# Kernel tuning notes

Hardware: AMD Instinct MI355X
Metric: run time of the kernel (lower is better)

Reference implementation:

```python
import jax, jax.numpy as jnp
import numpy as np

N = 100000
E = 1600000
G = 100
HEADS = 4
CH = 32
POS = 16
IN_DIM = 128
OUT_DIM = 64
NEG_SLOPE = 0.2
BN_EPS = 1e-5


def _grid_positions(batch):
    # replicate _get_normalized_positions: per-graph ceil(sqrt(count)) grid, vectorized
    counts = jax.ops.segment_sum(jnp.ones(N, jnp.int32), batch, num_segments=G)
    starts = jnp.concatenate([jnp.zeros(1, jnp.int32), jnp.cumsum(counts)[:-1].astype(jnp.int32)])
    local = jnp.arange(N, dtype=jnp.int32) - starts[batch]
    cnt = counts[batch]
    gs = jnp.ceil(jnp.sqrt(cnt.astype(jnp.float32))).astype(jnp.int32)
    row = local // gs
    col = local % gs
    denom = jnp.maximum(gs - 1, 1).astype(jnp.float32)
    return jnp.stack([row.astype(jnp.float32) / denom, col.astype(jnp.float32) / denom], axis=1)


def _seg_softmax(alpha, dst):
    # numerically-stable softmax over edges grouped by destination node
    amax = jax.ops.segment_max(alpha, dst, num_segments=N)
    amax = jnp.where(jnp.isfinite(amax), amax, 0.0)
    e = jnp.exp(alpha - amax[dst])
    s = jax.ops.segment_sum(e, dst, num_segments=N)
    return e / (s[dst] + 1e-16)


def _gat_layer(h, pos, src, dst, W, att, Wp, b):
    xt = (h @ W.T).reshape(N, HEADS, CH)                       # [N,H,C]
    pe = (pos[dst] - pos[src]) @ Wp.T                          # [E',P]
    a = att[0]                                                 # [H, 2C+P]
    # decompose (cat(x_src, x_dst, pe) * att).sum(-1) to avoid [E',H,2C+P] intermediate
    a_src = jnp.einsum('nhc,hc->nh', xt, a[:, :CH])
    a_dst = jnp.einsum('nhc,hc->nh', xt, a[:, CH:2 * CH])
    alpha = a_src[src] + a_dst[dst] + pe @ a[:, 2 * CH:].T     # [E',H]
    alpha = jnp.where(alpha > 0, alpha, NEG_SLOPE * alpha)     # leaky_relu
    alpha = _seg_softmax(alpha, dst)
    # faithful to source: message uses x[dst_idx], aggregated onto dst
    out = jax.ops.segment_sum(xt[dst] * alpha[:, :, None], dst, num_segments=N)
    return out.reshape(N, HEADS * CH) + b


def _batchnorm(h, g, b):
    mu = h.mean(0)
    var = h.var(0)  # biased, matches torch BN training-mode normalization
    return (h - mu) / jnp.sqrt(var + BN_EPS) * g + b


def setup_inputs() -> dict:
    key = jax.random.key(0)
    ks = jax.random.split(key, 20)
    s = 0.1
    return {
        'x': jax.random.normal(ks[0], (N, IN_DIM), jnp.float32),
        'edge_index': jax.random.randint(ks[1], (2, E), 0, N, jnp.int32),
        'batch': (jnp.arange(N, dtype=jnp.int32) // (N // G)).astype(jnp.int32),
        'pe_W': jax.random.normal(ks[2], (POS, 2), jnp.float32) * s,
        'pe_b': jax.random.normal(ks[3], (POS,), jnp.float32) * s,
        'lin_W0': jax.random.normal(ks[4], (HEADS * CH, IN_DIM + POS), jnp.float32) * s,
        'att0': jax.random.normal(ks[5], (1, HEADS, 2 * CH + POS), jnp.float32) * s,
        'posW0': jax.random.normal(ks[6], (POS, 2), jnp.float32) * s,
        'bias0': jax.random.normal(ks[7], (HEADS * CH,), jnp.float32) * s,
        'bn_g0': jax.random.uniform(ks[8], (HEADS * CH,), jnp.float32, 0.5, 1.5),
        'bn_b0': jax.random.normal(ks[9], (HEADS * CH,), jnp.float32) * s,
        'lin_W1': jax.random.normal(ks[10], (HEADS * CH, HEADS * CH), jnp.float32) * s,
        'att1': jax.random.normal(ks[11], (1, HEADS, 2 * CH + POS), jnp.float32) * s,
        'posW1': jax.random.normal(ks[12], (POS, 2), jnp.float32) * s,
        'bias1': jax.random.normal(ks[13], (HEADS * CH,), jnp.float32) * s,
        'bn_g1': jax.random.uniform(ks[14], (HEADS * CH,), jnp.float32, 0.5, 1.5),
        'bn_b1': jax.random.normal(ks[15], (HEADS * CH,), jnp.float32) * s,
        'fc_W': jax.random.normal(ks[16], (OUT_DIM, HEADS * CH), jnp.float32) * s,
        'fc_b': jax.random.normal(ks[17], (OUT_DIM,), jnp.float32) * s,
    }


def reference(x, edge_index, batch, pe_W, pe_b,
              lin_W0, att0, posW0, bias0, bn_g0, bn_b0,
              lin_W1, att1, posW1, bias1, bn_g1, bn_b1,
              fc_W, fc_b):
    pos = _grid_positions(batch)
    h = jnp.concatenate([x, pos @ pe_W.T + pe_b], axis=1)      # PositionalEncoding
    loop = jnp.arange(N, dtype=edge_index.dtype)
    src = jnp.concatenate([edge_index[0], loop])               # add_self_loops
    dst = jnp.concatenate([edge_index[1], loop])
    layers = ((lin_W0, att0, posW0, bias0, bn_g0, bn_b0),
              (lin_W1, att1, posW1, bias1, bn_g1, bn_b1))
    for (W, att, Wp, b, g, bb) in layers:
        h = _gat_layer(h, pos, src, dst, W, att, Wp, b)
        h = _batchnorm(h, g, bb)
        h = jax.nn.elu(h)
        # dropout: eval mode (identity); _refine_positions is identity
    counts = jax.ops.segment_sum(jnp.ones(N, jnp.float32), batch, num_segments=G)
    pooled = jax.ops.segment_sum(h, batch, num_segments=G) / counts[:, None]
    return pooled @ fc_W.T + fc_b
```

## Files before the change

kernel.cpp:

```cpp
#include <hip/hip_runtime.h>

#define NN 100000

typedef __bf16 bf16x8 __attribute__((ext_vector_type(8)));
typedef float  f32x4  __attribute__((ext_vector_type(4)));

__device__ __forceinline__ float b2f(ushort u) {
    union { unsigned int i; float f; } v; v.i = ((unsigned int)u) << 16; return v.f;
}
__device__ __forceinline__ ushort f2b(float f) {
    union { float f; unsigned int i; } v; v.f = f;
    unsigned int r = (v.i + 0x7fffu + ((v.i >> 16) & 1u)) >> 16;
    return (ushort)r;
}
__device__ __forceinline__ float elu_f(float v) {
    return v > 0.0f ? v : __expf(v) - 1.0f;
}

__global__ __launch_bounds__(256)
void zero_k(const float* __restrict__ W0, const float* __restrict__ W1,
            float* __restrict__ stats, float* __restrict__ out,
            ushort* __restrict__ wb0, ushort* __restrict__ wb1) {
    int i = blockIdx.x * 256 + threadIdx.x;
    if (i < 14592) { if (i < 8192) stats[i] = 0.0f; else out[i - 8192] = 0.0f; }
    if (i < 18432) wb0[i] = f2b(W0[i]);
    else if (i < 34816) wb1[i - 18432] = f2b(W1[i - 18432]);
}

template<int KK, int KP, bool FIRST>
__global__ __launch_bounds__(256, 4)
void gemm_k(const void* __restrict__ Av, const ushort* __restrict__ Wb,
            const float* __restrict__ peW, const float* __restrict__ peB,
            const float* __restrict__ statsIn, const float* __restrict__ g,
            const float* __restrict__ bb, ushort* __restrict__ Z,
            float* __restrict__ statsOut)
{
    constexpr int NKC = KP / 32;
    __shared__ ushort ZS[64 * 136];
    __shared__ float smS[256], smQ[256];
    __shared__ float smSS[256];
    const int t = threadIdx.x;
    const int blockM = blockIdx.x * 64;

    const int wave = t >> 6, lane = t & 63;
    const int wm = (wave & 1) * 32, wn = (wave >> 1) * 64;
    const int m = lane & 15, kq = lane >> 4;

    bf16x8 af[2][NKC];
    if constexpr (FIRST) {
        const float* A = (const float*)Av;
        #pragma unroll
        for (int mi = 0; mi < 2; ++mi) {
            const int gr = blockM + wm + mi * 16 + m;
            const bool ok = gr < NN;
            #pragma unroll
            for (int kc = 0; kc < 4; ++kc) {
                const int k0 = kc * 32 + kq * 8;
                float4 v0 = make_float4(0.f, 0.f, 0.f, 0.f), v1 = v0;
                if (ok) {
                    v0 = *(const float4*)(A + (size_t)gr * 128 + k0);
                    v1 = *(const float4*)(A + (size_t)gr * 128 + k0 + 4);
                }
                ushort u[8] = { f2b(v0.x), f2b(v0.y), f2b(v0.z), f2b(v0.w),
                                f2b(v1.x), f2b(v1.y), f2b(v1.z), f2b(v1.w) };
                af[mi][kc] = *(bf16x8*)u;
            }
            {
                ushort u[8] = {0, 0, 0, 0, 0, 0, 0, 0};
                if (kq < 2 && ok) {
                    const int local = gr - (gr / 1000) * 1000;
                    const float px = (float)(local >> 5) * (1.0f / 31.0f);
                    const float py = (float)(local & 31) * (1.0f / 31.0f);
                    #pragma unroll
                    for (int j = 0; j < 8; ++j) {
                        int p = kq * 8 + j;
                        u[j] = f2b(px * peW[2 * p] + py * peW[2 * p + 1] + peB[p]);
                    }
                }
                af[mi][NKC - 1] = *(bf16x8*)u;
            }
        }
    } else {
        const ushort* A = (const ushort*)Av;
        uint4 raw[2][4];
        #pragma unroll
        for (int mi = 0; mi < 2; ++mi) {
            const int gr = blockM + wm + mi * 16 + m;
            const bool ok = gr < NN;
            #pragma unroll
            for (int kc = 0; kc < 4; ++kc) {
                raw[mi][kc] = make_uint4(0u, 0u, 0u, 0u);
                if (ok) raw[mi][kc] = *(const uint4*)(A + (size_t)gr * 128 + kc * 32 + kq * 8);
            }
        }
        if (t < 128) {
            float S = 0.f, Q = 0.f;
            #pragma unroll
            for (int k = 0; k < 16; ++k) {
                S += statsIn[k * 256 + t]; Q += statsIn[k * 256 + 128 + t];
            }
            float mu = S * (1.0f / NN);
            float var = fmaxf(Q * (1.0f / NN) - mu * mu, 0.0f);
            float istd = rsqrtf(var + 1e-5f);
            float sc = g[t] * istd;
            smSS[t] = sc; smSS[128 + t] = bb[t] - mu * sc;
        }
        __syncthreads();
        #pragma unroll
        for (int mi = 0; mi < 2; ++mi) {
            const bool ok = (blockM + wm + mi * 16 + m) < NN;
            #pragma unroll
            for (int kc = 0; kc < 4; ++kc) {
                const int k0 = kc * 32 + kq * 8;
                ushort* u = (ushort*)&raw[mi][kc];
                #pragma unroll
                for (int j = 0; j < 8; ++j) {
                    float val = b2f(u[j]) * smSS[k0 + j] + smSS[128 + k0 + j];
                    u[j] = ok ? f2b(elu_f(val)) : (ushort)0;
                }
                af[mi][kc] = *(bf16x8*)&raw[mi][kc];
            }
        }
    }

    f32x4 acc[2][4];
    #pragma unroll
    for (int mi = 0; mi < 2; ++mi)
        #pragma unroll
        for (int ni = 0; ni < 4; ++ni)
            acc[mi][ni] = (f32x4){0.0f, 0.0f, 0.0f, 0.0f};

    #pragma unroll
    for (int kc = 0; kc < NKC; ++kc) {
        const int k0 = kc * 32 + kq * 8;
        bf16x8 bf[4];
        #pragma unroll
        for (int ni = 0; ni < 4; ++ni) {
            if (KP == KK || k0 < KK)
                bf[ni] = *(const bf16x8*)(Wb + (wn + ni * 16 + m) * KK + k0);
            else {
                ushort z[8] = {0, 0, 0, 0, 0, 0, 0, 0};
                bf[ni] = *(bf16x8*)z;
            }
        }
        #pragma unroll
        for (int mi = 0; mi < 2; ++mi)
            #pragma unroll
            for (int ni = 0; ni < 4; ++ni)
                acc[mi][ni] = __builtin_amdgcn_mfma_f32_16x16x32_bf16(
                    af[mi][kc], bf[ni], acc[mi][ni], 0, 0, 0);
    }

    float s[4] = {0, 0, 0, 0}, q[4] = {0, 0, 0, 0};
    #pragma unroll
    for (int mi = 0; mi < 2; ++mi)
        #pragma unroll
        for (int ni = 0; ni < 4; ++ni)
            #pragma unroll
            for (int r = 0; r < 4; ++r) {
                const float z = acc[mi][ni][r];
                s[ni] += z; q[ni] += z * z;
            }
    #pragma unroll
    for (int ni = 0; ni < 4; ++ni) {
        s[ni] += __shfl_xor(s[ni], 16); s[ni] += __shfl_xor(s[ni], 32);
        q[ni] += __shfl_xor(q[ni], 16); q[ni] += __shfl_xor(q[ni], 32);
    }
    if (lane < 16) {
        #pragma unroll
        for (int ni = 0; ni < 4; ++ni) {
            const int idx = wave * 64 + ni * 16 + m;
            smS[idx] = s[ni]; smQ[idx] = q[ni];
        }
    }
    #pragma unroll
    for (int mi = 0; mi < 2; ++mi)
        #pragma unroll
        for (int ni = 0; ni < 4; ++ni) {
            const int col = wn + ni * 16 + m;
            const int rb = wm + mi * 16 + kq * 4;
            #pragma unroll
            for (int r = 0; r < 4; ++r)
                ZS[(rb + r) * 136 + col] = f2b(acc[mi][ni][r]);
        }
    __syncthreads();

    if (t < 128) {
        const int base = (t >> 6) * 128 + (t & 63);
        float S = smS[base] + smS[base + 64];
        float Q = smQ[base] + smQ[base + 64];
        float* sl = statsOut + (blockIdx.x & 15) * 256;
        atomicAdd(sl + t, S);
        atomicAdd(sl + 128 + t, Q);
    }
    #pragma unroll
    for (int i = 0; i < 4; ++i) {
        const int idx = i * 256 + t;
        const int row = idx >> 4, c16 = idx & 15;
        const int gr = blockM + row;
        if (gr < NN)
            *(uint4*)(Z + (size_t)gr * 128 + c16 * 8) =
                *(const uint4*)(ZS + row * 136 + c16 * 8);
    }
}

__global__ __launch_bounds__(256)
void poolfc_k(const ushort* __restrict__ Z, const float* __restrict__ stats,
              const float* __restrict__ g, const float* __restrict__ bb,
              const float* __restrict__ fcW, const float* __restrict__ fcB,
              float* __restrict__ out) {
    __shared__ float smSS[256];
    __shared__ float smT[16 * 128];
    __shared__ float smP[128];
    const int t = threadIdx.x;
    if (t < 128) {
        float S = 0.f, Q = 0.f;
        #pragma unroll
        for (int k = 0; k < 16; ++k) { S += stats[k * 256 + t]; Q += stats[k * 256 + 128 + t]; }
        float mu = S * (1.0f / NN);
        float var = fmaxf(Q * (1.0f / NN) - mu * mu, 0.0f);
        float istd = rsqrtf(var + 1e-5f);
        float sc = g[t] * istd;
        smSS[t] = sc; smSS[128 + t] = bb[t] - mu * sc;
    }
    __syncthreads();
    const int gg = blockIdx.x >> 2, part = blockIdx.x & 3;
    const int r16 = t >> 4, c8 = t & 15;
    const int r0 = gg * 1000 + part * 250;
    float sc[8], sh[8];
    #pragma unroll
    for (int j = 0; j < 8; ++j) { sc[j] = smSS[c8 * 8 + j]; sh[j] = smSS[128 + c8 * 8 + j]; }
    float a[8] = {0, 0, 0, 0, 0, 0, 0, 0};
    #pragma unroll
    for (int i = 0; i < 16; ++i) {
        if (i < 15 || r16 < 10) {
            const uint4 v = *(const uint4*)(Z + ((size_t)(r0 + i * 16 + r16)) * 128 + c8 * 8);
            const ushort* u = (const ushort*)&v;
            #pragma unroll
            for (int j = 0; j < 8; ++j) a[j] += elu_f(b2f(u[j]) * sc[j] + sh[j]);
        }
    }
    #pragma unroll
    for (int j = 0; j < 8; ++j) smT[r16 * 128 + c8 * 8 + j] = a[j];
    __syncthreads();
    if (t < 128) {
        float S = 0.0f;
        #pragma unroll
        for (int k = 0; k < 16; ++k) S += smT[k * 128 + t];
        smP[t] = S;
    }
    __syncthreads();
    if (t < 64) {
        float d = 0.0f;
        #pragma unroll
        for (int j4 = 0; j4 < 32; ++j4) {
            float4 w = *(const float4*)(fcW + t * 128 + j4 * 4);
            d += smP[j4 * 4 + 0] * w.x + smP[j4 * 4 + 1] * w.y
               + smP[j4 * 4 + 2] * w.z + smP[j4 * 4 + 3] * w.w;
        }
        float acc = d * (1.0f / 1000.0f) + (part == 0 ? fcB[t] : 0.0f);
        atomicAdd(&out[gg * 64 + t], acc);
    }
}

extern "C" void kernel_launch(void* const* d_in, const int* in_sizes, int n_in,
                              void* d_out, int out_size, void* d_ws, size_t ws_size,
                              hipStream_t stream) {
    const float* x   = (const float*)d_in[0];
    const float* peW = (const float*)d_in[3];
    const float* peB = (const float*)d_in[4];
    const float* W0  = (const float*)d_in[5];
    const float* g0  = (const float*)d_in[9];
    const float* bb0 = (const float*)d_in[10];
    const float* W1  = (const float*)d_in[11];
    const float* g1  = (const float*)d_in[15];
    const float* bb1 = (const float*)d_in[16];
    const float* fcW = (const float*)d_in[17];
    const float* fcB = (const float*)d_in[18];
    float* out = (float*)d_out;

    float* wsF = (float*)d_ws;
    float* stats1 = wsF;
    float* stats2 = wsF + 4096;
    ushort* wb0 = (ushort*)((char*)d_ws + 65536);
    ushort* wb1 = (ushort*)((char*)d_ws + 131072);
    ushort* z1 = (ushort*)((char*)d_ws + 262144);
    ushort* z2 = (ushort*)((char*)d_ws + 25862144);

    zero_k<<<136, 256, 0, stream>>>(W0, W1, stats1, out, wb0, wb1);
    gemm_k<144, 160, true ><<<1563, 256, 0, stream>>>(
        (const void*)x, wb0, peW, peB, nullptr, nullptr, nullptr, z1, stats1);
    gemm_k<128, 128, false><<<1563, 256, 0, stream>>>(
        (const void*)z1, wb1, nullptr, nullptr, stats1, g0, bb0, z2, stats2);
    poolfc_k<<<400, 256, 0, stream>>>(z2, stats2, g1, bb1, fcW, fcB, out);
}
```

Baseline: 183.8 us.

## Recompute first GEMM to fuse BN+ELU into second GEMM, dropping intermediate buffer

Result: slower. 190.9 us (+3.9%).

```diff
diff --git a/kernel.cpp b/kernel.cpp
--- a/kernel.cpp
+++ b/kernel.cpp
@@ -27,152 +27,209 @@
     else if (i < 34816) wb1[i - 18432] = f2b(W1[i - 18432]);
 }
 
-template<int KK, int KP, bool FIRST>
-__global__ __launch_bounds__(256, 4)
-void gemm_k(const void* __restrict__ Av, const ushort* __restrict__ Wb,
-            const float* __restrict__ peW, const float* __restrict__ peB,
-            const float* __restrict__ statsIn, const float* __restrict__ g,
-            const float* __restrict__ bb, ushort* __restrict__ Z,
-            float* __restrict__ statsOut)
+__device__ __forceinline__ void build_af(bf16x8 af[2][5], const float* __restrict__ x,
+                                         const float* __restrict__ peW,
+                                         const float* __restrict__ peB,
+                                         int blockM, int wm, int m, int kq) {
+    #pragma unroll
+    for (int mi = 0; mi < 2; ++mi) {
+        const int gr = blockM + wm + mi * 16 + m;
+        const bool ok = gr < NN;
+        #pragma unroll
+        for (int kc = 0; kc < 4; ++kc) {
+            const int k0 = kc * 32 + kq * 8;
+            float4 v0 = make_float4(0.f, 0.f, 0.f, 0.f), v1 = v0;
+            if (ok) {
+                v0 = *(const float4*)(x + (size_t)gr * 128 + k0);
+                v1 = *(const float4*)(x + (size_t)gr * 128 + k0 + 4);
+            }
+            ushort u[8] = { f2b(v0.x), f2b(v0.y), f2b(v0.z), f2b(v0.w),
+                            f2b(v1.x), f2b(v1.y), f2b(v1.z), f2b(v1.w) };
+            af[mi][kc] = *(bf16x8*)u;
+        }
+        {
+            ushort u[8] = {0, 0, 0, 0, 0, 0, 0, 0};
+            if (kq < 2 && ok) {
+                const int local = gr - (gr / 1000) * 1000;
+                const float px = (float)(local >> 5) * (1.0f / 31.0f);
+                const float py = (float)(local & 31) * (1.0f / 31.0f);
+                #pragma unroll
+                for (int j = 0; j < 8; ++j) {
+                    int p = kq * 8 + j;
+                    u[j] = f2b(px * peW[2 * p] + py * peW[2 * p + 1] + peB[p]);
+                }
+            }
+            af[mi][4] = *(bf16x8*)u;
+        }
+    }
+}
+
+__device__ __forceinline__ void mfma_s1(f32x4 acc[2][4], bf16x8 af[2][5],
+                                        const ushort* __restrict__ wb0,
+                                        int wn, int m, int kq) {
+    #pragma unroll
+    for (int kc = 0; kc < 5; ++kc) {
+        const int k0 = kc * 32 + kq * 8;
+        bf16x8 bf[4];
+        #pragma unroll
+        for (int ni = 0; ni < 4; ++ni) {
+            if (k0 < 144)
+                bf[ni] = *(const bf16x8*)(wb0 + (wn + ni * 16 + m) * 144 + k0);
+            else {
+                ushort z[8] = {0, 0, 0, 0, 0, 0, 0, 0};
+                bf[ni] = *(bf16x8*)z;
+            }
+        }
+        #pragma unroll
+        for (int mi = 0; mi < 2; ++mi)
+            #pragma unroll
+            for (int ni = 0; ni < 4; ++ni)
+                acc[mi][ni] = __builtin_amdgcn_mfma_f32_16x16x32_bf16(
+                    af[mi][kc], bf[ni], acc[mi][ni], 0, 0, 0);
+    }
+}
+
+__device__ __forceinline__ void stats_epi(const f32x4 acc[2][4], float* smS, float* smQ,
+                                          float* __restrict__ statsOut,
+                                          int t, int wave, int lane, int wn, int m,
+                                          int bid) {
+    float s[4] = {0, 0, 0, 0}, q[4] = {0, 0, 0, 0};
+    #pragma unroll
+    for (int mi = 0; mi < 2; ++mi)
+        #pragma unroll
+        for (int ni = 0; ni < 4; ++ni)
+            #pragma unroll
+            for (int r = 0; r < 4; ++r) {
+                const float z = acc[mi][ni][r];
+                s[ni] += z; q[ni] += z * z;
+            }
+    #pragma unroll
+    for (int ni = 0; ni < 4; ++ni) {
+        s[ni] += __shfl_xor(s[ni], 16); s[ni] += __shfl_xor(s[ni], 32);
+        q[ni] += __shfl_xor(q[ni], 16); q[ni] += __shfl_xor(q[ni], 32);
+    }
+    if (lane < 16) {
+        #pragma unroll
+        for (int ni = 0; ni < 4; ++ni) {
+            const int idx = wave * 64 + ni * 16 + m;
+            smS[idx] = s[ni]; smQ[idx] = q[ni];
+        }
+    }
+    __syncthreads();
+    if (t < 128) {
+        const int base = (t >> 6) * 128 + (t & 63);
+        float S = smS[base] + smS[base + 64];
+        float Q = smQ[base] + smQ[base + 64];
+        float* sl = statsOut + (bid & 15) * 256;
+        atomicAdd(sl + t, S);
+        atomicAdd(sl + 128 + t, Q);
+    }
+}
+
+__global__ __launch_bounds__(256)
+void gemm1s_k(const float* __restrict__ x, const ushort* __restrict__ wb0,
+              const float* __restrict__ peW, const float* __restrict__ peB,
+              float* __restrict__ stats1)
 {
-    constexpr int NKC = KP / 32;
-    __shared__ ushort ZS[64 * 136];
+    __shared__ float smS[256], smQ[256];
+    const int t = threadIdx.x;
+    const int blockM = blockIdx.x * 64;
+    const int wave = t >> 6, lane = t & 63;
+    const int wm = (wave & 1) * 32, wn = (wave >> 1) * 64;
+    const int m = lane & 15, kq = lane >> 4;
+
+    bf16x8 af[2][5];
+    build_af(af, x, peW, peB, blockM, wm, m, kq);
+    f32x4 acc[2][4];
+    #pragma unroll
+    for (int mi = 0; mi < 2; ++mi)
+        #pragma unroll
+        for (int ni = 0; ni < 4; ++ni) acc[mi][ni] = (f32x4){0.f, 0.f, 0.f, 0.f};
+    mfma_s1(acc, af, wb0, wn, m, kq);
+    stats_epi(acc, smS, smQ, stats1, t, wave, lane, wn, m, blockIdx.x);
+}
+
+__global__ __launch_bounds__(256, 2)
+void gemm2f_k(const float* __restrict__ x, const ushort* __restrict__ wb0,
+              const ushort* __restrict__ wb1,
+              const float* __restrict__ peW, const float* __restrict__ peB,
+              const float* __restrict__ stats1, const float* __restrict__ g0,
+              const float* __restrict__ bb0, ushort* __restrict__ Z,
+              float* __restrict__ stats2)
+{
+    __shared__ ushort h1S[64 * 136];
     __shared__ float smS[256], smQ[256];
     __shared__ float smSS[256];
     const int t = threadIdx.x;
     const int blockM = blockIdx.x * 64;
-
     const int wave = t >> 6, lane = t & 63;
     const int wm = (wave & 1) * 32, wn = (wave >> 1) * 64;
     const int m = lane & 15, kq = lane >> 4;
 
-    bf16x8 af[2][NKC];
-    if constexpr (FIRST) {
-        const float* A = (const float*)Av;
-        #pragma unroll
-        for (int mi = 0; mi < 2; ++mi) {
-            const int gr = blockM + wm + mi * 16 + m;
-            const bool ok = gr < NN;
-            #pragma unroll
-            for (int kc = 0; kc < 4; ++kc) {
-                const int k0 = kc * 32 + kq * 8;
-                float4 v0 = make_float4(0.f, 0.f, 0.f, 0.f), v1 = v0;
-                if (ok) {
-                    v0 = *(const float4*)(A + (size_t)gr * 128 + k0);
-                    v1 = *(const float4*)(A + (size_t)gr * 128 + k0 + 4);
-                }
-                ushort u[8] = { f2b(v0.x), f2b(v0.y), f2b(v0.z), f2b(v0.w),
-                                f2b(v1.x), f2b(v1.y), f2b(v1.z), f2b(v1.w) };
-                af[mi][kc] = *(bf16x8*)u;
-            }
-            {
-                ushort u[8] = {0, 0, 0, 0, 0, 0, 0, 0};
-                if (kq < 2 && ok) {
-                    const int local = gr - (gr / 1000) * 1000;
-                    const float px = (float)(local >> 5) * (1.0f / 31.0f);
-                    const float py = (float)(local & 31) * (1.0f / 31.0f);
-                    #pragma unroll
-                    for (int j = 0; j < 8; ++j) {
-                        int p = kq * 8 + j;
-                        u[j] = f2b(px * peW[2 * p] + py * peW[2 * p + 1] + peB[p]);
-                    }
-                }
-                af[mi][NKC - 1] = *(bf16x8*)u;
-            }
-        }
-    } else {
-        const ushort* A = (const ushort*)Av;
-        uint4 raw[2][4];
-        #pragma unroll
-        for (int mi = 0; mi < 2; ++mi) {
-            const int gr = blockM + wm + mi * 16 + m;
-            const bool ok = gr < NN;
-            #pragma unroll
-            for (int kc = 0; kc < 4; ++kc) {
-                raw[mi][kc] = make_uint4(0u, 0u, 0u, 0u);
-                if (ok) raw[mi][kc] = *(const uint4*)(A + (size_t)gr * 128 + kc * 32 + kq * 8);
-            }
-        }
-        if (t < 128) {
-            float S = 0.f, Q = 0.f;
-            #pragma unroll
-            for (int k = 0; k < 16; ++k) {
-                S += statsIn[k * 256 + t]; Q += statsIn[k * 256 + 128 + t];
-            }
-            float mu = S * (1.0f / NN);
-            float var = fmaxf(Q * (1.0f / NN) - mu * mu, 0.0f);
-            float istd = rsqrtf(var + 1e-5f);
-            float sc = g[t] * istd;
-            smSS[t] = sc; smSS[128 + t] = bb[t] - mu * sc;
-        }
-        __syncthreads();
-        #pragma unroll
-        for (int mi = 0; mi < 2; ++mi) {
-            const bool ok = (blockM + wm + mi * 16 + m) < NN;
-            #pragma unroll
-            for (int kc = 0; kc < 4; ++kc) {
-                const int k0 = kc * 32 + kq * 8;
-                ushort* u = (ushort*)&raw[mi][kc];
-                #pragma unroll
-                for (int j = 0; j < 8; ++j) {
-                    float val = b2f(u[j]) * smSS[k0 + j] + smSS[128 + k0 + j];
-                    u[j] = ok ? f2b(elu_f(val)) : (ushort)0;
-                }
-                af[mi][kc] = *(bf16x8*)&raw[mi][kc];
-            }
-        }
-    }
-
-    f32x4 acc[2][4];
-    #pragma unroll
-    for (int mi = 0; mi < 2; ++mi)
+    if (t < 128) {
+        float S = 0.f, Q = 0.f;
+        #pragma unroll
+        for (int k = 0; k < 16; ++k) { S += stats1[k * 256 + t]; Q += stats1[k * 256 + 128 + t]; }
+        float mu = S * (1.0f / NN);
+        float var = fmaxf(Q * (1.0f / NN) - mu * mu, 0.0f);
+        float istd = rsqrtf(var + 1e-5f);
+        float sc = g0[t] * istd;
+        smSS[t] = sc; smSS[128 + t] = bb0[t] - mu * sc;
+    }
+
+    bf16x8 af[2][5];
+    build_af(af, x, peW, peB, blockM, wm, m, kq);
+    f32x4 acc1[2][4];
+    #pragma unroll
+    for (int mi = 0; mi < 2; ++mi)
+        #pragma unroll
+        for (int ni = 0; ni < 4; ++ni) acc1[mi][ni] = (f32x4){0.f, 0.f, 0.f, 0.f};
+    mfma_s1(acc1, af, wb0, wn, m, kq);
+
+    __syncthreads();
+
+    #pragma unroll
+    for (int mi = 0; mi < 2; ++mi)
+        #pragma unroll
+        for (int ni = 0; ni < 4; ++ni) {
+            const int col = wn + ni * 16 + m;
+            const float sc = smSS[col], sh = smSS[128 + col];
+            const int rb = wm + mi * 16 + kq * 4;
+            #pragma unroll
+            for (int r = 0; r < 4; ++r) {
+                const bool ok = (blockM + rb + r) < NN;
+                const float h = elu_f(acc1[mi][ni][r] * sc + sh);
+                h1S[(rb + r) * 136 + col] = ok ? f2b(h) : (ushort)0;
+            }
+        }
+    __syncthreads();
+
+    f32x4 acc2[2][4];
+    #pragma unroll
+    for (int mi = 0; mi < 2; ++mi)
+        #pragma unroll
+        for (int ni = 0; ni < 4; ++ni) acc2[mi][ni] = (f32x4){0.f, 0.f, 0.f, 0.f};
+    #pragma unroll
+    for (int kc = 0; kc < 4; ++kc) {
+        const int k0 = kc * 32 + kq * 8;
+        bf16x8 a2[2], bf[4];
+        #pragma unroll
+        for (int mi = 0; mi < 2; ++mi)
+            a2[mi] = *(const bf16x8*)(h1S + (wm + mi * 16 + m) * 136 + k0);
         #pragma unroll
         for (int ni = 0; ni < 4; ++ni)
-            acc[mi][ni] = (f32x4){0.0f, 0.0f, 0.0f, 0.0f};
-
-    #pragma unroll
-    for (int kc = 0; kc < NKC; ++kc) {
-        const int k0 = kc * 32 + kq * 8;
-        bf16x8 bf[4];
-        #pragma unroll
-        for (int ni = 0; ni < 4; ++ni) {
-            if (KP == KK || k0 < KK)
-                bf[ni] = *(const bf16x8*)(Wb + (wn + ni * 16 + m) * KK + k0);
-            else {
-                ushort z[8] = {0, 0, 0, 0, 0, 0, 0, 0};
-                bf[ni] = *(bf16x8*)z;
-            }
-        }
+            bf[ni] = *(const bf16x8*)(wb1 + (wn + ni * 16 + m) * 128 + k0);
         #pragma unroll
         for (int mi = 0; mi < 2; ++mi)
             #pragma unroll
             for (int ni = 0; ni < 4; ++ni)
-                acc[mi][ni] = __builtin_amdgcn_mfma_f32_16x16x32_bf16(
-                    af[mi][kc], bf[ni], acc[mi][ni], 0, 0, 0);
-    }
-
-    float s[4] = {0, 0, 0, 0}, q[4] = {0, 0, 0, 0};
-    #pragma unroll
-    for (int mi = 0; mi < 2; ++mi)
-        #pragma unroll
-        for (int ni = 0; ni < 4; ++ni)
-            #pragma unroll
-            for (int r = 0; r < 4; ++r) {
-                const float z = acc[mi][ni][r];
-                s[ni] += z; q[ni] += z * z;
-            }
-    #pragma unroll
-    for (int ni = 0; ni < 4; ++ni) {
-        s[ni] += __shfl_xor(s[ni], 16); s[ni] += __shfl_xor(s[ni], 32);
-        q[ni] += __shfl_xor(q[ni], 16); q[ni] += __shfl_xor(q[ni], 32);
-    }
-    if (lane < 16) {
-        #pragma unroll
-        for (int ni = 0; ni < 4; ++ni) {
-            const int idx = wave * 64 + ni * 16 + m;
-            smS[idx] = s[ni]; smQ[idx] = q[ni];
-        }
-    }
+                acc2[mi][ni] = __builtin_amdgcn_mfma_f32_16x16x32_bf16(
+                    a2[mi], bf[ni], acc2[mi][ni], 0, 0, 0);
+    }
+
+    stats_epi(acc2, smS, smQ, stats2, t, wave, lane, wn, m, blockIdx.x);
+
+    ushort* ZS = h1S;
     #pragma unroll
     for (int mi = 0; mi < 2; ++mi)
         #pragma unroll
@@ -181,18 +238,9 @@
             const int rb = wm + mi * 16 + kq * 4;
             #pragma unroll
             for (int r = 0; r < 4; ++r)
-                ZS[(rb + r) * 136 + col] = f2b(acc[mi][ni][r]);
-        }
-    __syncthreads();
-
-    if (t < 128) {
-        const int base = (t >> 6) * 128 + (t & 63);
-        float S = smS[base] + smS[base + 64];
-        float Q = smQ[base] + smQ[base + 64];
-        float* sl = statsOut + (blockIdx.x & 15) * 256;
-        atomicAdd(sl + t, S);
-        atomicAdd(sl + 128 + t, Q);
-    }
+                ZS[(rb + r) * 136 + col] = f2b(acc2[mi][ni][r]);
+        }
+    __syncthreads();
     #pragma unroll
     for (int i = 0; i < 4; ++i) {
         const int idx = i * 256 + t;
@@ -284,13 +332,11 @@
     float* stats2 = wsF + 4096;
     ushort* wb0 = (ushort*)((char*)d_ws + 65536);
     ushort* wb1 = (ushort*)((char*)d_ws + 131072);
-    ushort* z1 = (ushort*)((char*)d_ws + 262144);
-    ushort* z2 = (ushort*)((char*)d_ws + 25862144);
+    ushort* z2 = (ushort*)((char*)d_ws + 262144);
 
     zero_k<<<136, 256, 0, stream>>>(W0, W1, stats1, out, wb0, wb1);
-    gemm_k<144, 160, true ><<<1563, 256, 0, stream>>>(
-        (const void*)x, wb0, peW, peB, nullptr, nullptr, nullptr, z1, stats1);
-    gemm_k<128, 128, false><<<1563, 256, 0, stream>>>(
-        (const void*)z1, wb1, nullptr, nullptr, stats1, g0, bb0, z2, stats2);
+    gemm1s_k<<<1563, 256, 0, stream>>>(x, wb0, peW, peB, stats1);
+    gemm2f_k<<<1563, 256, 0, stream>>>(x, wb0, wb1, peW, peB,
+                                       stats1, g0, bb0, z2, stats2);
     poolfc_k<<<400, 256, 0, stream>>>(z2, stats2, g1, bb1, fcW, fcB, out);
 }
```
